# Kernel tuning notes

Measured on AMD Instinct MI355X. Metric: run time of the kernel, lower is better.

Reference implementation:

```python
import jax, jax.numpy as jnp
import numpy as np

B = 4            # batch size (coords[:,0].max()+1 in the original)
C = 64           # NUM_BEV_FEATURES
NX, NY, NZ = 432, 496, 1
P_PER = 16000    # pillars per sample per bin
N_BINS = 3       # intersweep_sequence_length


def _make_coords(seed):
    # unique BEV cells per sample: strided modular arange (stride coprime with NX*NY)
    stride = 9973
    cells = (np.arange(P_PER, dtype=np.int64)[None, :] * stride + 17 * seed + 31 * np.arange(B)[:, None]) % (NX * NY)
    y = (cells // NX).reshape(-1)
    x = (cells % NX).reshape(-1)
    b = np.repeat(np.arange(B, dtype=np.int64), P_PER)
    z = np.zeros_like(b)
    return jnp.asarray(np.stack([b, z, y, x], axis=1), dtype=jnp.int32)  # [B*P_PER, 4]


def setup_inputs() -> dict:
    key = jax.random.key(0)
    inp = {}
    for i in range(N_BINS):
        key, kf = jax.random.split(key)
        inp[f"pillar_features_bin_{i}"] = jax.random.normal(kf, (B * P_PER, C), dtype=jnp.float32)
        inp[f"voxel_coords_bin_{i}"] = _make_coords(i)
    return inp


def _scatter_bin(pillars, coords):
    # coords layout: [batch, z, y, x]; per-sample flat index = z + y*nx + x (nz==1)
    c = coords.astype(jnp.int32)
    flat = c[:, 0] * (NY * NX) + c[:, 1] + c[:, 2] * NX + c[:, 3]  # batch-offset flattened index
    canvas = jnp.zeros((B * NY * NX, C), dtype=pillars.dtype).at[flat].set(pillars)
    return canvas.reshape(B, NY, NX, C).transpose(0, 3, 1, 2)  # [B, C, NY, NX]


def reference(pillar_features_bin_0, voxel_coords_bin_0,
              pillar_features_bin_1, voxel_coords_bin_1,
              pillar_features_bin_2, voxel_coords_bin_2):
    out0 = _scatter_bin(pillar_features_bin_0, voxel_coords_bin_0)
    out1 = _scatter_bin(pillar_features_bin_1, voxel_coords_bin_1)
    out2 = _scatter_bin(pillar_features_bin_2, voxel_coords_bin_2)
    return (out0, out1, out2)
```

## Files before the change

### kernel.cpp

```cpp
#include <hip/hip_runtime.h>

#define NX_ 432
#define NY_ 496
#define C_  64
#define B_  4
#define CELLS_ (NX_ * NY_)
#define PLANE_ ((size_t)CELLS_)
#define BATCH_STRIDE_ ((size_t)C_ * CELLS_)
#define BIN_STRIDE_   ((size_t)B_ * C_ * CELLS_)
#define MAP_BIN_ ((size_t)B_ * CELLS_)

typedef float vfloat4 __attribute__((ext_vector_type(4)));
typedef int   vint4   __attribute__((ext_vector_type(4)));

__global__ __launch_bounds__(256) void scatter_idx_kernel(
    const int* __restrict__ coords0,
    const int* __restrict__ coords1,
    const int* __restrict__ coords2,
    int* __restrict__ map, int npil)
{
    const int bin = blockIdx.y;
    const int p = blockIdx.x * 256 + threadIdx.x;
    if (p >= npil) return;
    const int* coords = (bin == 0) ? coords0 : (bin == 1) ? coords1 : coords2;
    vint4 c = ((const vint4*)coords)[p];
    size_t idx = (size_t)bin * MAP_BIN_ + (size_t)c.x * CELLS_ + c.y + c.z * NX_ + c.w;
    map[idx] = p;
}

__global__ __launch_bounds__(256) void gather_kernel(
    const float* __restrict__ pf0,
    const float* __restrict__ pf1,
    const float* __restrict__ pf2,
    const int* __restrict__ map,
    float* __restrict__ out)
{
    const int bin = blockIdx.z;
    const int b   = blockIdx.y;
    const int cell = blockIdx.x * 1024 + threadIdx.x * 4;
    if (cell >= CELLS_) return;

    const float* __restrict__ pf = (bin == 0) ? pf0 : (bin == 1) ? pf1 : pf2;

    const int* m = map + (size_t)bin * MAP_BIN_ + (size_t)b * CELLS_ + cell;
    vint4 idx = *(const vint4*)m;

    const bool v0 = idx.x >= 0, v1 = idx.y >= 0, v2 = idx.z >= 0, v3 = idx.w >= 0;
    const float* r0 = pf + (size_t)(v0 ? idx.x : 0) * C_;
    const float* r1 = pf + (size_t)(v1 ? idx.y : 0) * C_;
    const float* r2 = pf + (size_t)(v2 ? idx.z : 0) * C_;
    const float* r3 = pf + (size_t)(v3 ? idx.w : 0) * C_;

    float* o = out + (size_t)bin * BIN_STRIDE_ + (size_t)b * BATCH_STRIDE_ + cell;

#pragma unroll 4
    for (int c = 0; c < C_; ++c) {
        float x0 = r0[c];
        float x1 = r1[c];
        float x2 = r2[c];
        float x3 = r3[c];
        vfloat4 v;
        v.x = v0 ? x0 : 0.0f;
        v.y = v1 ? x1 : 0.0f;
        v.z = v2 ? x2 : 0.0f;
        v.w = v3 ? x3 : 0.0f;
        __builtin_nontemporal_store(v, (vfloat4*)(o + (size_t)c * PLANE_));
    }
}

extern "C" void kernel_launch(void* const* d_in, const int* in_sizes, int n_in,
                              void* d_out, int out_size, void* d_ws, size_t ws_size,
                              hipStream_t stream) {
    const float* pf0 = (const float*)d_in[0];
    const int*   co0 = (const int*)d_in[1];
    const float* pf1 = (const float*)d_in[2];
    const int*   co1 = (const int*)d_in[3];
    const float* pf2 = (const float*)d_in[4];
    const int*   co2 = (const int*)d_in[5];
    float* out = (float*)d_out;

    const int npil = in_sizes[1] / 4;

    int* map = (int*)d_ws;
    const size_t map_bytes = 3 * MAP_BIN_ * sizeof(int);

    (void)hipMemsetAsync(map, 0xFF, map_bytes, stream);

    dim3 g1((npil + 255) / 256, 3, 1);
    scatter_idx_kernel<<<g1, 256, 0, stream>>>(co0, co1, co2, map, npil);

    dim3 g2((CELLS_ + 1023) / 1024, B_, 3);
    gather_kernel<<<g2, 256, 0, stream>>>(pf0, pf1, pf2, map, out);
}
```

Before: 698.2 us.

## Restructure gather kernel to split channels into groups of four with vector row loads

The gather kernel's grid changes from (cell block, batch, bin) to (cell split, channel group of 4, batch*bin). Each block loops over a 1/16 slice of cells and handles only 4 channels. Each thread loads one float4 per pillar row instead of scalar loads, transposes the four vectors in registers and writes four channel planes. The map is now read 16 times, once per channel group, and each pillar row is touched by 16 blocks. In exchange, scalar row reads become vector loads and there are more, finer-grained blocks with looping.

```diff
diff --git a/kernel.cpp b/kernel.cpp
--- a/kernel.cpp
+++ b/kernel.cpp
@@ -9,6 +9,9 @@
 #define BATCH_STRIDE_ ((size_t)C_ * CELLS_)
 #define BIN_STRIDE_   ((size_t)B_ * C_ * CELLS_)
 #define MAP_BIN_ ((size_t)B_ * CELLS_)
+
+#define SPLITS_ 16
+#define SPLIT_CELLS_ (CELLS_ / SPLITS_)
 
 typedef float vfloat4 __attribute__((ext_vector_type(4)));
 typedef int   vint4   __attribute__((ext_vector_type(4)));
@@ -35,36 +38,43 @@
     const int* __restrict__ map,
     float* __restrict__ out)
 {
-    const int bin = blockIdx.z;
-    const int b   = blockIdx.y;
-    const int cell = blockIdx.x * 1024 + threadIdx.x * 4;
-    if (cell >= CELLS_) return;
+    const int split = blockIdx.x;
+    const int c4    = blockIdx.y;
+    const int bb    = blockIdx.z;
+    const int bin = bb >> 2;
+    const int b   = bb & 3;
 
     const float* __restrict__ pf = (bin == 0) ? pf0 : (bin == 1) ? pf1 : pf2;
+    const float* __restrict__ pfc = pf + c4 * 4;
 
-    const int* m = map + (size_t)bin * MAP_BIN_ + (size_t)b * CELLS_ + cell;
-    vint4 idx = *(const vint4*)m;
+    const int* mbase = map + (size_t)bin * MAP_BIN_ + (size_t)b * CELLS_
+                           + (size_t)split * SPLIT_CELLS_;
+    float* obase = out + (size_t)bin * BIN_STRIDE_ + (size_t)b * BATCH_STRIDE_
+                       + (size_t)(c4 * 4) * PLANE_ + (size_t)split * SPLIT_CELLS_;
 
-    const bool v0 = idx.x >= 0, v1 = idx.y >= 0, v2 = idx.z >= 0, v3 = idx.w >= 0;
-    const float* r0 = pf + (size_t)(v0 ? idx.x : 0) * C_;
-    const float* r1 = pf + (size_t)(v1 ? idx.y : 0) * C_;
-    const float* r2 = pf + (size_t)(v2 ? idx.z : 0) * C_;
-    const float* r3 = pf + (size_t)(v3 ? idx.w : 0) * C_;
+    for (int base = threadIdx.x * 4; base < SPLIT_CELLS_; base += 1024) {
+        vint4 idx = *(const vint4*)(mbase + base);
+        const bool v0 = idx.x >= 0, v1 = idx.y >= 0, v2 = idx.z >= 0, v3 = idx.w >= 0;
 
-    float* o = out + (size_t)bin * BIN_STRIDE_ + (size_t)b * BATCH_STRIDE_ + cell;
+        vfloat4 a0 = *(const vfloat4*)(pfc + (size_t)(v0 ? idx.x : 0) * C_);
+        vfloat4 a1 = *(const vfloat4*)(pfc + (size_t)(v1 ? idx.y : 0) * C_);
+        vfloat4 a2 = *(const vfloat4*)(pfc + (size_t)(v2 ? idx.z : 0) * C_);
+        vfloat4 a3 = *(const vfloat4*)(pfc + (size_t)(v3 ? idx.w : 0) * C_);
 
-#pragma unroll 4
-    for (int c = 0; c < C_; ++c) {
-        float x0 = r0[c];
-        float x1 = r1[c];
-        float x2 = r2[c];
-        float x3 = r3[c];
-        vfloat4 v;
-        v.x = v0 ? x0 : 0.0f;
-        v.y = v1 ? x1 : 0.0f;
-        v.z = v2 ? x2 : 0.0f;
-        v.w = v3 ? x3 : 0.0f;
-        __builtin_nontemporal_store(v, (vfloat4*)(o + (size_t)c * PLANE_));
+        a0 = v0 ? a0 : (vfloat4)0.0f;
+        a1 = v1 ? a1 : (vfloat4)0.0f;
+        a2 = v2 ? a2 : (vfloat4)0.0f;
+        a3 = v3 ? a3 : (vfloat4)0.0f;
+
+        vfloat4 w0 = {a0.x, a1.x, a2.x, a3.x};
+        vfloat4 w1 = {a0.y, a1.y, a2.y, a3.y};
+        vfloat4 w2 = {a0.z, a1.z, a2.z, a3.z};
+        vfloat4 w3 = {a0.w, a1.w, a2.w, a3.w};
+
+        __builtin_nontemporal_store(w0, (vfloat4*)(obase + 0 * PLANE_ + base));
+        __builtin_nontemporal_store(w1, (vfloat4*)(obase + 1 * PLANE_ + base));
+        __builtin_nontemporal_store(w2, (vfloat4*)(obase + 2 * PLANE_ + base));
+        __builtin_nontemporal_store(w3, (vfloat4*)(obase + 3 * PLANE_ + base));
     }
 }
 
@@ -89,6 +99,6 @@
     dim3 g1((npil + 255) / 256, 3, 1);
     scatter_idx_kernel<<<g1, 256, 0, stream>>>(co0, co1, co2, map, npil);
 
-    dim3 g2((CELLS_ + 1023) / 1024, B_, 3);
+    dim3 g2(SPLITS_, 16, 12);
     gather_kernel<<<g2, 256, 0, stream>>>(pf0, pf1, pf2, map, out);
 }
```

Result: slower. 729.1 us (+4.4%).

## Stage gathered pillar rows in LDS tile and transpose for coalesced channel-plane writes

Applied to the files above, without the earlier changes.

The gather kernel now processes 216-cell chunks per block. It compacts the occupied cells into an LDS list and has each wave load a whole 64-float pillar row coalesced into a padded LDS tile. The tile is then written out as channel-plane float4 nontemporal stores. This replaces four scattered strided row reads per thread with coalesced row reads and skips loads for empty cells, at the cost of LDS zeroing, two extra barriers and about 55KB of LDS per block, which limits occupancy. The pillar index is packed into 16 bits, which holds only while each bin has at most 65536 pillars.

```diff
diff --git a/kernel.cpp b/kernel.cpp
--- a/kernel.cpp
+++ b/kernel.cpp
@@ -9,6 +9,11 @@
 #define BATCH_STRIDE_ ((size_t)C_ * CELLS_)
 #define BIN_STRIDE_   ((size_t)B_ * C_ * CELLS_)
 #define MAP_BIN_ ((size_t)B_ * CELLS_)
+
+#define TCELLS_  216
+#define NCHUNK_  992
+#define TSTRIDE_ 217
+#define TFLOATS_ (C_ * TCELLS_)
 
 typedef float vfloat4 __attribute__((ext_vector_type(4)));
 typedef int   vint4   __attribute__((ext_vector_type(4)));
@@ -28,43 +33,61 @@
     map[idx] = p;
 }
 
-__global__ __launch_bounds__(256) void gather_kernel(
+__global__ __launch_bounds__(256) void gather_lds_kernel(
     const float* __restrict__ pf0,
     const float* __restrict__ pf1,
     const float* __restrict__ pf2,
     const int* __restrict__ map,
     float* __restrict__ out)
 {
-    const int bin = blockIdx.z;
-    const int b   = blockIdx.y;
-    const int cell = blockIdx.x * 1024 + threadIdx.x * 4;
-    if (cell >= CELLS_) return;
+    __shared__ float tile[C_ * TSTRIDE_];
+    __shared__ unsigned list[256];
+    __shared__ int cnt;
+
+    const int chunk = blockIdx.x;
+    const int b     = blockIdx.y;
+    const int bin   = blockIdx.z;
+    const int tid   = threadIdx.x;
 
     const float* __restrict__ pf = (bin == 0) ? pf0 : (bin == 1) ? pf1 : pf2;
 
-    const int* m = map + (size_t)bin * MAP_BIN_ + (size_t)b * CELLS_ + cell;
-    vint4 idx = *(const vint4*)m;
+    {
+        vfloat4 z = {0.0f, 0.0f, 0.0f, 0.0f};
+        vfloat4* t4 = (vfloat4*)tile;
+        #pragma unroll
+        for (int i = tid; i < (C_ * TSTRIDE_) / 4; i += 256) t4[i] = z;
+    }
+    if (tid == 0) cnt = 0;
+    __syncthreads();
 
-    const bool v0 = idx.x >= 0, v1 = idx.y >= 0, v2 = idx.z >= 0, v3 = idx.w >= 0;
-    const float* r0 = pf + (size_t)(v0 ? idx.x : 0) * C_;
-    const float* r1 = pf + (size_t)(v1 ? idx.y : 0) * C_;
-    const float* r2 = pf + (size_t)(v2 ? idx.z : 0) * C_;
-    const float* r3 = pf + (size_t)(v3 ? idx.w : 0) * C_;
+    if (tid < TCELLS_) {
+        int p = map[(size_t)bin * MAP_BIN_ + (size_t)b * CELLS_
+                    + (size_t)chunk * TCELLS_ + tid];
+        if (p >= 0) {
+            int pos = atomicAdd(&cnt, 1);
+            list[pos] = ((unsigned)tid << 16) | (unsigned)p;
+        }
+    }
+    __syncthreads();
 
-    float* o = out + (size_t)bin * BIN_STRIDE_ + (size_t)b * BATCH_STRIDE_ + cell;
+    const int wave = tid >> 6, lane = tid & 63;
+    const int n = cnt;
+    for (int e = wave; e < n; e += 4) {
+        unsigned ent = list[e];
+        int cell = (int)(ent >> 16);
+        int p    = (int)(ent & 0xFFFFu);
+        tile[lane * TSTRIDE_ + cell] = pf[(size_t)p * C_ + lane];
+    }
+    __syncthreads();
 
-#pragma unroll 4
-    for (int c = 0; c < C_; ++c) {
-        float x0 = r0[c];
-        float x1 = r1[c];
-        float x2 = r2[c];
-        float x3 = r3[c];
-        vfloat4 v;
-        v.x = v0 ? x0 : 0.0f;
-        v.y = v1 ? x1 : 0.0f;
-        v.z = v2 ? x2 : 0.0f;
-        v.w = v3 ? x3 : 0.0f;
-        __builtin_nontemporal_store(v, (vfloat4*)(o + (size_t)c * PLANE_));
+    float* obase = out + (size_t)bin * BIN_STRIDE_ + (size_t)b * BATCH_STRIDE_
+                       + (size_t)chunk * TCELLS_;
+    for (int flat = tid * 4; flat < TFLOATS_; flat += 1024) {
+        int c    = flat / TCELLS_;
+        int cell = flat - c * TCELLS_;
+        const float* src = tile + c * TSTRIDE_ + cell;
+        vfloat4 v = {src[0], src[1], src[2], src[3]};
+        __builtin_nontemporal_store(v, (vfloat4*)(obase + (size_t)c * PLANE_ + cell));
     }
 }
 
@@ -89,6 +112,6 @@
     dim3 g1((npil + 255) / 256, 3, 1);
     scatter_idx_kernel<<<g1, 256, 0, stream>>>(co0, co1, co2, map, npil);
 
-    dim3 g2((CELLS_ + 1023) / 1024, B_, 3);
-    gather_kernel<<<g2, 256, 0, stream>>>(pf0, pf1, pf2, map, out);
+    dim3 g2(NCHUNK_, B_, 3);
+    gather_lds_kernel<<<g2, 256, 0, stream>>>(pf0, pf1, pf2, map, out);
 }
```

Result: slower. 740.5 us (+6.0%).
